# Optimization experiments

Hardware: AMD Instinct MI355X
Metric: run time of the kernel (lower is better)

## Reference

```python
import jax, jax.numpy as jnp
import numpy as np

FEATURE_SIZE = 40960
ACCUM_SIZE = 512
L1_SIZE = 32
L2_SIZE = 32
BATCH = 4096
SPARSITY = 30.0 / FEATURE_SIZE  # ~30 active features per position (HalfKP-like)


def screlu(x):
    # Squared Clipped ReLU: clamp(x, 0, 1)^2
    return jnp.square(jnp.clip(x, 0.0, 1.0))


def setup_inputs() -> dict:
    key = jax.random.key(0)
    ks = jax.random.split(key, 12)
    # sparse binary feature planes, ~30 active per row
    wf = (jax.random.uniform(ks[0], (BATCH, FEATURE_SIZE)) < SPARSITY).astype(jnp.float32)
    bf = (jax.random.uniform(ks[1], (BATCH, FEATURE_SIZE)) < SPARSITY).astype(jnp.float32)
    stm = jax.random.randint(ks[2], (BATCH,), 0, 2).astype(jnp.bool_)

    def lin(kw, kb, fan_in, fan_out):
        bound = 1.0 / np.sqrt(fan_in)
        w = jax.random.uniform(kw, (fan_out, fan_in), minval=-bound, maxval=bound, dtype=jnp.float32)
        b = jax.random.uniform(kb, (fan_out,), minval=-bound, maxval=bound, dtype=jnp.float32)
        return w, b

    ft_w, ft_b = lin(ks[3], ks[4], FEATURE_SIZE, ACCUM_SIZE)
    l1_w, l1_b = lin(ks[5], ks[6], ACCUM_SIZE * 2, L1_SIZE)
    l2_w, l2_b = lin(ks[7], ks[8], L1_SIZE, L2_SIZE)
    out_w, out_b = lin(ks[9], ks[10], L2_SIZE, 1)
    return {
        "white_features": wf, "black_features": bf, "stm": stm,
        "ft_w": ft_w, "ft_b": ft_b,
        "l1_w": l1_w, "l1_b": l1_b,
        "l2_w": l2_w, "l2_b": l2_b,
        "out_w": out_w, "out_b": out_b,
    }


def reference(white_features, black_features, stm,
              ft_w, ft_b, l1_w, l1_b, l2_w, l2_b, out_w, out_b):
    # feature transformer (sparse gather-accumulate expressed as GEMM) + screlu
    w_accum = screlu(white_features @ ft_w.T + ft_b)  # [B, A]
    b_accum = screlu(black_features @ ft_w.T + ft_b)  # [B, A]
    stm_mask = stm[:, None]
    stm_accum = jnp.where(stm_mask, b_accum, w_accum)
    nstm_accum = jnp.where(stm_mask, w_accum, b_accum)
    x = jnp.concatenate([stm_accum, nstm_accum], axis=1)  # [B, 2A]
    v = screlu(x @ l1_w.T + l1_b)
    v = screlu(v @ l2_w.T + l2_b)
    value = (v @ out_w.T + out_b)[:, 0]  # [B]
    return value
```

## Files before the change

### kernel.cpp

```cpp
#include <hip/hip_runtime.h>

#define FEATS 40960
#define ACC 512
#define NBATCH 4096
#define CAP 192

__device__ __forceinline__ float screlu_f(float v) {
  v = fminf(fmaxf(v, 0.0f), 1.0f);
  return v * v;
}

__global__ __launch_bounds__(256) void transpose_ftw(const float* __restrict__ w,
                                                     float* __restrict__ wt) {
  __shared__ float tile[64][65];
  const int f0 = blockIdx.x * 64;
  const int o0 = blockIdx.y * 64;
  const int tx = threadIdx.x & 63;
  const int ty = threadIdx.x >> 6;
#pragma unroll
  for (int i = 0; i < 16; ++i) {
    const int o = ty * 16 + i;
    tile[o][tx] = w[(size_t)(o0 + o) * FEATS + (f0 + tx)];
  }
  __syncthreads();
#pragma unroll
  for (int i = 0; i < 16; ++i) {
    const int f = ty * 16 + i;
    wt[(size_t)(f0 + f) * ACC + (o0 + tx)] = tile[tx][f];
  }
}

__global__ __launch_bounds__(256) void nnue_fused(
    const float* __restrict__ wfeat, const float* __restrict__ bfeat,
    const unsigned char* __restrict__ stm8,
    const float* __restrict__ wt, const float* __restrict__ ftb,
    const float* __restrict__ l1w, const float* __restrict__ l1b,
    const float* __restrict__ l2w, const float* __restrict__ l2b,
    const float* __restrict__ ow, const float* __restrict__ ob,
    float* __restrict__ out)
{
  __shared__ int wcnt, bcnt, u8flag;
  __shared__ int widx[CAP], bidx[CAP];
  __shared__ __align__(16) float x[1024];
  __shared__ float part[8][32];
  __shared__ float v1[32];

  const int t = threadIdx.x;
  const int row = blockIdx.x;

  if (t == 0) { wcnt = 0; bcnt = 0; u8flag = 0; }
  __syncthreads();

  if (stm8[4 * t + 1] != 0) u8flag = 1;

  const uint4* w4 = (const uint4*)(wfeat + (size_t)row * FEATS);
  const uint4* b4 = (const uint4*)(bfeat + (size_t)row * FEATS);
  for (int i = t; i < FEATS / 4; i += 256) {
    const uint4 a = w4[i];
    if (a.x | a.y | a.z | a.w) {
      if (a.x) { int p = atomicAdd(&wcnt, 1); if (p < CAP) widx[p] = 4 * i + 0; }
      if (a.y) { int p = atomicAdd(&wcnt, 1); if (p < CAP) widx[p] = 4 * i + 1; }
      if (a.z) { int p = atomicAdd(&wcnt, 1); if (p < CAP) widx[p] = 4 * i + 2; }
      if (a.w) { int p = atomicAdd(&wcnt, 1); if (p < CAP) widx[p] = 4 * i + 3; }
    }
    const uint4 b = b4[i];
    if (b.x | b.y | b.z | b.w) {
      if (b.x) { int p = atomicAdd(&bcnt, 1); if (p < CAP) bidx[p] = 4 * i + 0; }
      if (b.y) { int p = atomicAdd(&bcnt, 1); if (p < CAP) bidx[p] = 4 * i + 1; }
      if (b.z) { int p = atomicAdd(&bcnt, 1); if (p < CAP) bidx[p] = 4 * i + 2; }
      if (b.w) { int p = atomicAdd(&bcnt, 1); if (p < CAP) bidx[p] = 4 * i + 3; }
    }
  }
  __syncthreads();

  const int nw = min(wcnt, CAP);
  const int nb = min(bcnt, CAP);
  float accwx = 0.f, accwy = 0.f, accbx = 0.f, accby = 0.f;
  const float2* wt2 = (const float2*)wt;
  for (int i = 0; i < nw; ++i) {
    const float2 v = wt2[(size_t)widx[i] * (ACC / 2) + t];
    accwx += v.x; accwy += v.y;
  }
  for (int i = 0; i < nb; ++i) {
    const float2 v = wt2[(size_t)bidx[i] * (ACC / 2) + t];
    accbx += v.x; accby += v.y;
  }
  const float2 bias = ((const float2*)ftb)[t];
  accwx = screlu_f(accwx + bias.x); accwy = screlu_f(accwy + bias.y);
  accbx = screlu_f(accbx + bias.x); accby = screlu_f(accby + bias.y);

  const int stm = (u8flag != 0) ? (int)stm8[row] : ((const int*)stm8)[row];
  const int woff = stm ? 512 : 0;
  const int boff = 512 - woff;
  x[woff + 2 * t]     = accwx;
  x[woff + 2 * t + 1] = accwy;
  x[boff + 2 * t]     = accbx;
  x[boff + 2 * t + 1] = accby;
  __syncthreads();

  const int o = t & 31, c = t >> 5;
  const float4* lw4 = (const float4*)(l1w + (size_t)o * 1024 + c * 128);
  const float4* x4  = (const float4*)(x) + c * 32;
  float s = 0.f;
#pragma unroll
  for (int i = 0; i < 32; ++i) {
    const float4 wv = lw4[i];
    const float4 xv = x4[i];
    s += wv.x * xv.x + wv.y * xv.y + wv.z * xv.z + wv.w * xv.w;
  }
  part[c][o] = s;
  __syncthreads();

  if (t < 32) {
    float r = l1b[t];
#pragma unroll
    for (int cc = 0; cc < 8; ++cc) r += part[cc][t];
    v1[t] = screlu_f(r);
  }
  __syncthreads();

  if (t < 32) {
    float r = l2b[t];
#pragma unroll
    for (int k = 0; k < 32; ++k) r += l2w[t * 32 + k] * v1[k];
    float res = screlu_f(r) * ow[t];
#pragma unroll
    for (int off = 16; off; off >>= 1) res += __shfl_down(res, off, 32);
    if (t == 0) out[row] = res + ob[0];
  }
}

extern "C" void kernel_launch(void* const* d_in, const int* in_sizes, int n_in,
                              void* d_out, int out_size, void* d_ws, size_t ws_size,
                              hipStream_t stream) {
  const float* wfeat = (const float*)d_in[0];
  const float* bfeat = (const float*)d_in[1];
  const unsigned char* stm = (const unsigned char*)d_in[2];
  const float* ftw = (const float*)d_in[3];
  const float* ftb = (const float*)d_in[4];
  const float* l1w = (const float*)d_in[5];
  const float* l1b = (const float*)d_in[6];
  const float* l2w = (const float*)d_in[7];
  const float* l2b = (const float*)d_in[8];
  const float* ow  = (const float*)d_in[9];
  const float* ob  = (const float*)d_in[10];
  float* out = (float*)d_out;
  float* wt  = (float*)d_ws;

  dim3 tgrid(FEATS / 64, ACC / 64);
  transpose_ftw<<<tgrid, dim3(256), 0, stream>>>(ftw, wt);
  nnue_fused<<<dim3(NBATCH), dim3(256), 0, stream>>>(
      wfeat, bfeat, stm, wt, ftb, l1w, l1b, l2w, l2b, ow, ob, out);
}
```

Before: 1.370 ms.

## Split sparse index extraction into a separate per-color kernel

Moves the scan of the dense feature planes out of the fused kernel into its own kernel launched on a (batch, color) grid. Each block scans only one color, doubling the number of blocks doing the scan, and writes counts and indices to workspace. The MLP kernel then reads the compact index lists instead of scanning 40960 floats per color. This adds a launch, extra workspace traffic for the indices, and relies on the workspace being large enough past the transposed weights.

```diff
diff --git a/kernel.cpp b/kernel.cpp
--- a/kernel.cpp
+++ b/kernel.cpp
@@ -9,6 +9,10 @@
   v = fminf(fmaxf(v, 0.0f), 1.0f);
   return v * v;
 }
+
+#define WT_ELEMS ((size_t)FEATS * ACC)
+#define WT_BYTES (WT_ELEMS * 4)
+#define CNT_BYTES ((size_t)2 * NBATCH * 4)
 
 __global__ __launch_bounds__(256) void transpose_ftw(const float* __restrict__ w,
                                                      float* __restrict__ wt) {
@@ -30,8 +34,39 @@
   }
 }
 
-__global__ __launch_bounds__(256) void nnue_fused(
+__global__ __launch_bounds__(256) void extract_idx(
     const float* __restrict__ wfeat, const float* __restrict__ bfeat,
+    int* __restrict__ cnts, int* __restrict__ idxs)
+{
+  __shared__ int cnt;
+  __shared__ int lidx[CAP];
+  const int row = blockIdx.x;
+  const int color = blockIdx.y;
+  const int t = threadIdx.x;
+  if (t == 0) cnt = 0;
+  __syncthreads();
+
+  const float* feat = color ? bfeat : wfeat;
+  const uint4* f4 = (const uint4*)(feat + (size_t)row * FEATS);
+  for (int i = t; i < FEATS / 4; i += 256) {
+    const uint4 a = f4[i];
+    if (a.x | a.y | a.z | a.w) {
+      if (a.x) { int p = atomicAdd(&cnt, 1); if (p < CAP) lidx[p] = 4 * i + 0; }
+      if (a.y) { int p = atomicAdd(&cnt, 1); if (p < CAP) lidx[p] = 4 * i + 1; }
+      if (a.z) { int p = atomicAdd(&cnt, 1); if (p < CAP) lidx[p] = 4 * i + 2; }
+      if (a.w) { int p = atomicAdd(&cnt, 1); if (p < CAP) lidx[p] = 4 * i + 3; }
+    }
+  }
+  __syncthreads();
+
+  const int cid = color * NBATCH + row;
+  const int n = min(cnt, CAP);
+  if (t == 0) cnts[cid] = n;
+  for (int i = t; i < n; i += 256) idxs[(size_t)cid * CAP + i] = lidx[i];
+}
+
+__global__ __launch_bounds__(256) void nnue_mlp(
+    const int* __restrict__ cnts, const int* __restrict__ idxs,
     const unsigned char* __restrict__ stm8,
     const float* __restrict__ wt, const float* __restrict__ ftb,
     const float* __restrict__ l1w, const float* __restrict__ l1b,
@@ -39,7 +74,7 @@
     const float* __restrict__ ow, const float* __restrict__ ob,
     float* __restrict__ out)
 {
-  __shared__ int wcnt, bcnt, u8flag;
+  __shared__ int u8flag;
   __shared__ int widx[CAP], bidx[CAP];
   __shared__ __align__(16) float x[1024];
   __shared__ float part[8][32];
@@ -48,33 +83,17 @@
   const int t = threadIdx.x;
   const int row = blockIdx.x;
 
-  if (t == 0) { wcnt = 0; bcnt = 0; u8flag = 0; }
+  if (t == 0) u8flag = 0;
   __syncthreads();
 
   if (stm8[4 * t + 1] != 0) u8flag = 1;
 
-  const uint4* w4 = (const uint4*)(wfeat + (size_t)row * FEATS);
-  const uint4* b4 = (const uint4*)(bfeat + (size_t)row * FEATS);
-  for (int i = t; i < FEATS / 4; i += 256) {
-    const uint4 a = w4[i];
-    if (a.x | a.y | a.z | a.w) {
-      if (a.x) { int p = atomicAdd(&wcnt, 1); if (p < CAP) widx[p] = 4 * i + 0; }
-      if (a.y) { int p = atomicAdd(&wcnt, 1); if (p < CAP) widx[p] = 4 * i + 1; }
-      if (a.z) { int p = atomicAdd(&wcnt, 1); if (p < CAP) widx[p] = 4 * i + 2; }
-      if (a.w) { int p = atomicAdd(&wcnt, 1); if (p < CAP) widx[p] = 4 * i + 3; }
-    }
-    const uint4 b = b4[i];
-    if (b.x | b.y | b.z | b.w) {
-      if (b.x) { int p = atomicAdd(&bcnt, 1); if (p < CAP) bidx[p] = 4 * i + 0; }
-      if (b.y) { int p = atomicAdd(&bcnt, 1); if (p < CAP) bidx[p] = 4 * i + 1; }
-      if (b.z) { int p = atomicAdd(&bcnt, 1); if (p < CAP) bidx[p] = 4 * i + 2; }
-      if (b.w) { int p = atomicAdd(&bcnt, 1); if (p < CAP) bidx[p] = 4 * i + 3; }
-    }
-  }
+  const int nw = min(cnts[row], CAP);
+  const int nb = min(cnts[NBATCH + row], CAP);
+  for (int i = t; i < nw; i += 256) widx[i] = idxs[(size_t)row * CAP + i];
+  for (int i = t; i < nb; i += 256) bidx[i] = idxs[(size_t)(NBATCH + row) * CAP + i];
   __syncthreads();
 
-  const int nw = min(wcnt, CAP);
-  const int nb = min(bcnt, CAP);
   float accwx = 0.f, accwy = 0.f, accbx = 0.f, accby = 0.f;
   const float2* wt2 = (const float2*)wt;
   for (int i = 0; i < nw; ++i) {
@@ -145,10 +164,13 @@
   const float* ow  = (const float*)d_in[9];
   const float* ob  = (const float*)d_in[10];
   float* out = (float*)d_out;
+
   float* wt  = (float*)d_ws;
+  int*   cnts = (int*)((char*)d_ws + WT_BYTES);
+  int*   idxs = (int*)((char*)d_ws + WT_BYTES + CNT_BYTES);
 
-  dim3 tgrid(FEATS / 64, ACC / 64);
-  transpose_ftw<<<tgrid, dim3(256), 0, stream>>>(ftw, wt);
-  nnue_fused<<<dim3(NBATCH), dim3(256), 0, stream>>>(
-      wfeat, bfeat, stm, wt, ftb, l1w, l1b, l2w, l2b, ow, ob, out);
+  extract_idx<<<dim3(NBATCH, 2), dim3(256), 0, stream>>>(wfeat, bfeat, cnts, idxs);
+  transpose_ftw<<<dim3(FEATS / 64, ACC / 64), dim3(256), 0, stream>>>(ftw, wt);
+  nnue_mlp<<<dim3(NBATCH), dim3(256), 0, stream>>>(
+      cnts, idxs, stm, wt, ftb, l1w, l1b, l2w, l2b, ow, ob, out);
 }
```

Measured after the change: 1.375 ms. About the same (+0.4%).
